# Kernel optimization log

Measured on AMD Instinct MI355X. Metric: run time of the kernel, lower is better.

## Reference

```python
import jax, jax.numpy as jnp
import numpy as np

N = 100000; E = 1000000; D = 192; FD = 64; L = 6; MLP = 192
TW = 768; NPD = 6; CPD = 7; TEMP = 0.5; NREL = 2; EPS = 1e-5


def _ln(x, g, b):
    mu = jnp.mean(x, axis=-1, keepdims=True)
    var = jnp.mean(jnp.square(x - mu), axis=-1, keepdims=True)
    return (x - mu) * jax.lax.rsqrt(var + EPS) * g + b


def _bn(x, g, b):
    # BatchNorm1d in training mode: batch statistics over the N (node) axis
    mu = jnp.mean(x, axis=0, keepdims=True)
    var = jnp.mean(jnp.square(x - mu), axis=0, keepdims=True)
    return (x - mu) * jax.lax.rsqrt(var + EPS) * g + b


def _rgcn(x, Wrel, Wroot, bias, src, dst, etype):
    # PyG RGCNConv, aggr='mean': out_i = x_i @ Wroot + b + sum_r mean_{j in N_r(i)} x_j @ W_r
    out = x @ Wroot + bias
    for r in range(NREL):
        h = x @ Wrel[r]                                   # [N, D] per-relation transform
        mask = (etype == r)
        msg = jnp.where(mask[:, None], jnp.take(h, src, axis=0), 0.0)  # [E, D]
        agg = jax.ops.segment_sum(msg, dst, num_segments=N)
        cnt = jax.ops.segment_sum(mask.astype(x.dtype), dst, num_segments=N)
        out = out + agg / jnp.maximum(cnt, 1.0)[:, None]
    return out


def _forward(tweet, num_prop, comments_prop,
             Wt, bt, Wn, bnum, Wc, bc,
             Wv, bv, Wo, bo, ln1_g, ln1_b, bn_g, bn_b,
             W1, b1, W2, b2, ln2_g, ln2_b,
             Wrel, Wroot, rgcn_b, Wm1, bm1, Wm2, bm2, Wm3, bm3,
             edge_index, edge_type, labels, train_idx):
    lrelu = jax.nn.leaky_relu  # negative_slope=0.01, same as torch LeakyReLU default
    t = lrelu(tweet @ Wt + bt)
    n = lrelu(num_prop @ Wn + bnum)
    c = lrelu(comments_prop @ Wc + bc)
    x = jnp.concatenate([t, n, c], axis=1)  # [N, D]; seq dim of size 1 is elided
    for i in range(L):
        # MHA over seq_len=1: softmax over a single key is exactly 1, so
        # attn_out = out_proj(v_proj(x)); Q/K projections have zero effect/grad.
        v = x @ Wv[i] + bv[i]
        x = x + (v @ Wo[i] + bo[i])          # dropout in eval mode = identity
        x = _ln(x, ln1_g[i], ln1_b[i])
        x = _bn(x, bn_g[i], bn_b[i])
        f = lrelu(x @ W1[i] + b1[i]) @ W2[i] + b2[i]
        x = x + f
        x = _ln(x, ln2_g[i], ln2_b[i])
    # supervised contrastive loss on first train_idx nodes (train_idx static int)
    feat = x[:train_idx]
    lab = labels[:train_idx]
    fn = feat / jnp.linalg.norm(feat, axis=-1, keepdims=True)
    sim = (fn @ fn.T) / TEMP                              # [T, T]
    ex = jnp.exp(sim)
    match = (lab[:, None] == lab[None, :]).astype(x.dtype)
    closs = jnp.mean(-jnp.log(jnp.sum(match * ex, axis=1) / jnp.sum(ex, axis=1)))
    # two passes through the SAME (shared-weight) RGCN; dropout(p=0.1) eval = identity
    src, dst = edge_index[0], edge_index[1]
    h = _rgcn(x, Wrel, Wroot, rgcn_b, src, dst, edge_type)
    h = _rgcn(h, Wrel, Wroot, rgcn_b, src, dst, edge_type)
    h = lrelu(h @ Wm1 + bm1)
    h = lrelu(h @ Wm2 + bm2)
    logits = h @ Wm3 + bm3                                # [N, 2]
    return logits, closs


def setup_inputs() -> dict:
    key = jax.random.key(0)
    ks = iter(jax.random.split(key, 64))
    f32 = jnp.float32
    def p(*shape):
        fan_in = shape[-2] if len(shape) >= 2 else shape[-1]
        return jax.random.normal(next(ks), shape, f32) * (1.0 / np.sqrt(fan_in))
    inp = {
        'tweet': jax.random.normal(next(ks), (N, TW), f32),
        'num_prop': jax.random.normal(next(ks), (N, NPD), f32),
        'comments_prop': jax.random.normal(next(ks), (N, CPD), f32),
        'Wt': p(TW, FD), 'bt': jnp.zeros((FD,), f32),
        'Wn': p(NPD, FD), 'bnum': jnp.zeros((FD,), f32),
        'Wc': p(CPD, FD), 'bc': jnp.zeros((FD,), f32),
        'Wv': p(L, D, D), 'bv': jnp.zeros((L, D), f32),
        'Wo': p(L, D, D), 'bo': jnp.zeros((L, D), f32),
        'ln1_g': jnp.ones((L, D), f32), 'ln1_b': jnp.zeros((L, D), f32),
        'bn_g': jnp.ones((L, D), f32), 'bn_b': jnp.zeros((L, D), f32),
        'W1': p(L, D, MLP), 'b1': jnp.zeros((L, MLP), f32),
        'W2': p(L, MLP, D), 'b2': jnp.zeros((L, D), f32),
        'ln2_g': jnp.ones((L, D), f32), 'ln2_b': jnp.zeros((L, D), f32),
        'Wrel': p(NREL, D, D), 'Wroot': p(D, D), 'rgcn_b': jnp.zeros((D,), f32),
        'Wm1': p(D, MLP), 'bm1': jnp.zeros((MLP,), f32),
        'Wm2': p(MLP, D), 'bm2': jnp.zeros((D,), f32),
        'Wm3': p(D, 2), 'bm3': jnp.zeros((2,), f32),
        'edge_index': jax.random.randint(next(ks), (2, E), 0, N, jnp.int32),
        'edge_type': jax.random.randint(next(ks), (E,), 0, NREL, jnp.int32),
        'labels': jax.random.randint(next(ks), (N,), 0, 2, jnp.int32),
        'train_idx': 8192,
    }
    return inp


def reference(tweet, num_prop, comments_prop, Wt, bt, Wn, bnum, Wc, bc,
              Wv, bv, Wo, bo, ln1_g, ln1_b, bn_g, bn_b,
              W1, b1, W2, b2, ln2_g, ln2_b,
              Wrel, Wroot, rgcn_b, Wm1, bm1, Wm2, bm2, Wm3, bm3,
              edge_index, edge_type, labels, train_idx):
    return _forward(tweet, num_prop, comments_prop, Wt, bt, Wn, bnum, Wc, bc,
                    Wv, bv, Wo, bo, ln1_g, ln1_b, bn_g, bn_b,
                    W1, b1, W2, b2, ln2_g, ln2_b,
                    Wrel, Wroot, rgcn_b, Wm1, bm1, Wm2, bm2, Wm3, bm3,
                    edge_index, edge_type, labels, train_idx)
```

## Files before the change

kernel.cpp:

```cpp
#include <hip/hip_runtime.h>

#define NN 100000
#define EE 1000000
#define DDIM 192
#define NLAYER 6
#define TRAIN 8192
#define SLOPE 0.01f
#define EPS_LN 1e-5f
#define TOTSEG (2 * NN)
#define SCAN_NB 98

typedef float f32x4 __attribute__((ext_vector_type(4)));
typedef __bf16 bf16x8 __attribute__((ext_vector_type(8)));
typedef unsigned short ushort_t;
typedef unsigned int uint_t;

__device__ __forceinline__ float lrelu(float v) { return v > 0.0f ? v : SLOPE * v; }

__device__ __forceinline__ ushort_t f2bf(float f) {
    union { float f; uint_t u; } v; v.f = f;
    uint_t u = v.u;
    u += 0x7fffu + ((u >> 16) & 1u);
    return (ushort_t)(u >> 16);
}

__device__ __forceinline__ float bf2f(ushort_t b) {
    union { uint_t u; float f; } v; v.u = ((uint_t)b) << 16; return v.f;
}

__device__ __forceinline__ float wave_sum(float s) {
    #pragma unroll
    for (int off = 32; off > 0; off >>= 1) s += __shfl_down(s, off);
    return __shfl(s, 0);
}

__global__ __launch_bounds__(256) void prep_w(
    const float* __restrict__ Wt, const float* __restrict__ Wv,
    const float* __restrict__ Wo, const float* __restrict__ W1,
    const float* __restrict__ W2, const float* __restrict__ Wrel,
    const float* __restrict__ Wroot, const float* __restrict__ Wm1,
    const float* __restrict__ Wm2, ushort_t* __restrict__ WTt,
    ushort_t* __restrict__ WTs, ushort_t* __restrict__ WTg)
{
    const int bid = blockIdx.x;
    if (bid < 29 * 144) {
        const int mat = bid / 144;
        const int o = (bid % 144) * 256 + threadIdx.x;
        const float* src;
        if      (mat <  6) src = Wv   + (size_t)mat * 36864;
        else if (mat < 12) src = Wo   + (size_t)(mat - 6)  * 36864;
        else if (mat < 18) src = W1   + (size_t)(mat - 12) * 36864;
        else if (mat < 24) src = W2   + (size_t)(mat - 18) * 36864;
        else if (mat < 26) src = Wrel + (size_t)(mat - 24) * 36864;
        else if (mat == 26) src = Wroot;
        else if (mat == 27) src = Wm1;
        else                src = Wm2;
        const int m = o / 192, k = o - m * 192;
        const ushort_t b = f2bf(src[(size_t)k * 192 + m]);
        if (mat == 24 || mat == 25)
            WTg[(size_t)m * 576 + 192 + (mat - 24) * 192 + k] = b;
        else if (mat == 26)
            WTg[(size_t)m * 576 + k] = b;
        else
            WTs[(size_t)mat * 36864 + o] = b;
    } else {
        const int o = (bid - 29 * 144) * 256 + threadIdx.x;
        const int m = o / 768, k = o - m * 768;
        WTt[o] = f2bf(Wt[(size_t)k * 64 + m]);
    }
}

template <int NFRAG, bool BIAS, bool RELU>
__global__ __launch_bounds__(256) void gemm_mfma(
    const float* __restrict__ A, const ushort_t* __restrict__ WT,
    const float* __restrict__ bias, float* __restrict__ C,
    int n, int K, int ldc)
{
    __shared__ ushort_t As[128 * 32];
    __shared__ ushort_t Ws[NFRAG * 16 * 32];
    const int tid = threadIdx.x;
    const int lane = tid & 63, w = tid >> 6;
    const int quad = lane >> 4, l15 = lane & 15;
    const int row0 = blockIdx.x * 128;

    f32x4 acc[2][NFRAG];
    #pragma unroll
    for (int m = 0; m < 2; ++m)
        #pragma unroll
        for (int nf = 0; nf < NFRAG; ++nf)
            acc[m][nf] = (f32x4){0.f, 0.f, 0.f, 0.f};

    const int srow = tid >> 1, shalf = tid & 1;
    const bool arow_ok = (row0 + srow) < n;
    const float* aptr = A + (size_t)(row0 + srow) * K + shalf * 16;
    const int ktiles = K >> 5;

    float f[16];
    if (arow_ok) {
        const float4* p = (const float4*)aptr;
        #pragma unroll
        for (int i = 0; i < 4; ++i) {
            const float4 t4 = p[i];
            f[i * 4 + 0] = t4.x; f[i * 4 + 1] = t4.y;
            f[i * 4 + 2] = t4.z; f[i * 4 + 3] = t4.w;
        }
    } else {
        #pragma unroll
        for (int i = 0; i < 16; ++i) f[i] = 0.f;
    }

    for (int t = 0; t < ktiles; ++t) {
        const int k0 = t << 5;
        uint_t u[8];
        #pragma unroll
        for (int i = 0; i < 8; ++i)
            u[i] = (uint_t)f2bf(f[2 * i]) | ((uint_t)f2bf(f[2 * i + 1]) << 16);
        uint4* dsta = (uint4*)&As[srow * 32 + shalf * 16];
        dsta[0] = make_uint4(u[0], u[1], u[2], u[3]);
        dsta[1] = make_uint4(u[4], u[5], u[6], u[7]);

        #pragma unroll
        for (int s = tid; s < NFRAG * 64; s += 256) {
            const int col = s >> 2, part = s & 3;
            *(uint4*)&Ws[col * 32 + part * 8] =
                *(const uint4*)(WT + (size_t)col * K + k0 + part * 8);
        }
        __syncthreads();

        float fn_[16];
        const bool more = (t + 1 < ktiles);
        if (more) {
            if (arow_ok) {
                const float4* p = (const float4*)(aptr + k0 + 32);
                #pragma unroll
                for (int i = 0; i < 4; ++i) {
                    const float4 t4 = p[i];
                    fn_[i * 4 + 0] = t4.x; fn_[i * 4 + 1] = t4.y;
                    fn_[i * 4 + 2] = t4.z; fn_[i * 4 + 3] = t4.w;
                }
            } else {
                #pragma unroll
                for (int i = 0; i < 16; ++i) fn_[i] = 0.f;
            }
        }

        const bf16x8 a0 = *(const bf16x8*)&As[(w * 32 + l15) * 32 + quad * 8];
        const bf16x8 a1 = *(const bf16x8*)&As[(w * 32 + 16 + l15) * 32 + quad * 8];
        #pragma unroll
        for (int nf = 0; nf < NFRAG; ++nf) {
            const bf16x8 b = *(const bf16x8*)&Ws[(nf * 16 + l15) * 32 + quad * 8];
            acc[0][nf] = __builtin_amdgcn_mfma_f32_16x16x32_bf16(a0, b, acc[0][nf], 0, 0, 0);
            acc[1][nf] = __builtin_amdgcn_mfma_f32_16x16x32_bf16(a1, b, acc[1][nf], 0, 0, 0);
        }
        __syncthreads();
        if (more) {
            #pragma unroll
            for (int i = 0; i < 16; ++i) f[i] = fn_[i];
        }
    }

    #pragma unroll
    for (int m = 0; m < 2; ++m) {
        #pragma unroll
        for (int reg = 0; reg < 4; ++reg) {
            const int gr = row0 + w * 32 + m * 16 + quad * 4 + reg;
            if (gr >= n) continue;
            #pragma unroll
            for (int nf = 0; nf < NFRAG; ++nf) {
                const int col = nf * 16 + l15;
                float x = acc[m][nf][reg] + (BIAS ? bias[col] : 0.f);
                if (RELU) x = lrelu(x);
                C[(size_t)gr * ldc + col] = x;
            }
        }
    }
}

template <bool ABF, bool RELU1, bool RELU2, bool RES, bool LNORM, bool BN,
          bool BNSTAT, bool CF32, bool CBF>
__global__ __launch_bounds__(256, 2) void gemm2_mfma(
    const void* __restrict__ Ain, const ushort_t* __restrict__ wta,
    const float* __restrict__ bias1, const ushort_t* __restrict__ wtb,
    const float* __restrict__ bias2, const void* __restrict__ resin,
    float* __restrict__ C, ushort_t* __restrict__ Cbf,
    const float* __restrict__ bnsum, const float* __restrict__ bng,
    const float* __restrict__ bnb, float* __restrict__ bnacc,
    const float* __restrict__ lg, const float* __restrict__ lb, int n)
{
    constexpr int VST = 200;
    __shared__ ushort_t Vs[128 * VST];
    __shared__ ushort_t Ws[192 * 32];
    __shared__ float scs[DDIM], shs[DDIM];
    ushort_t* As = Vs;
    const int tid = threadIdx.x;
    const int lane = tid & 63, w = tid >> 6;
    const int quad = lane >> 4, l15 = lane & 15;
    const int row0 = blockIdx.x * 128;

    if constexpr (BN) {
        const float invN = 1.0f / (float)NN;
        for (int j = tid; j < DDIM; j += 256) {
            const float mu = bnsum[j] * invN;
            const float var = bnsum[DDIM + j] * invN - mu * mu;
            const float sc = bng[j] * rsqrtf(var + EPS_LN);
            scs[j] = sc;
            shs[j] = fmaf(-mu, sc, bnb[j]);
        }
        __syncthreads();
    }

    f32x4 acc[2][12];
    #pragma unroll
    for (int m = 0; m < 2; ++m)
        #pragma unroll
        for (int nf = 0; nf < 12; ++nf)
            acc[m][nf] = (f32x4){0.f, 0.f, 0.f, 0.f};

    const int srow = tid >> 1, shalf = tid & 1;
    const bool arow_ok = (row0 + srow) < n;
    const float*    aF = (const float*)Ain + (size_t)(row0 + srow) * DDIM + shalf * 16;
    const ushort_t* aB = (const ushort_t*)Ain + (size_t)(row0 + srow) * DDIM + shalf * 16;

    float f[16];
    uint4 ub[2];

    if constexpr (!ABF) {
        if (arow_ok) {
            const float4* p = (const float4*)aF;
            #pragma unroll
            for (int i = 0; i < 4; ++i) {
                const float4 t4 = p[i];
                f[i * 4 + 0] = t4.x; f[i * 4 + 1] = t4.y;
                f[i * 4 + 2] = t4.z; f[i * 4 + 3] = t4.w;
            }
        } else {
            #pragma unroll
            for (int i = 0; i < 16; ++i) f[i] = 0.f;
        }
    } else {
        if (arow_ok) {
            const uint4* p = (const uint4*)aB;
            ub[0] = p[0]; ub[1] = p[1];
        } else {
            ub[0] = make_uint4(0, 0, 0, 0); ub[1] = make_uint4(0, 0, 0, 0);
        }
    }

    #pragma unroll 1
    for (int t = 0; t < 6; ++t) {
        const int k0 = t << 5;
        uint4* dsta = (uint4*)&As[srow * 32 + shalf * 16];
        if constexpr (!ABF) {
            uint_t u[8];
            #pragma unroll
            for (int i = 0; i < 8; ++i)
                u[i] = (uint_t)f2bf(f[2 * i]) | ((uint_t)f2bf(f[2 * i + 1]) << 16);
            dsta[0] = make_uint4(u[0], u[1], u[2], u[3]);
            dsta[1] = make_uint4(u[4], u[5], u[6], u[7]);
        } else if constexpr (BN) {
            const float4* scp = (const float4*)&scs[k0 + shalf * 16];
            const float4* shp = (const float4*)&shs[k0 + shalf * 16];
            const uint_t* uw = (const uint_t*)ub;
            uint_t u[8];
            #pragma unroll
            for (int i = 0; i < 4; ++i) {
                const float4 sc = scp[i], sh = shp[i];
                float x0 = bf2f((ushort_t)(uw[2 * i] & 0xffffu));
                float x1 = bf2f((ushort_t)(uw[2 * i] >> 16));
                float x2 = bf2f((ushort_t)(uw[2 * i + 1] & 0xffffu));
                float x3 = bf2f((ushort_t)(uw[2 * i + 1] >> 16));
                x0 = fmaf(x0, sc.x, sh.x); x1 = fmaf(x1, sc.y, sh.y);
                x2 = fmaf(x2, sc.z, sh.z); x3 = fmaf(x3, sc.w, sh.w);
                u[2 * i]     = (uint_t)f2bf(x0) | ((uint_t)f2bf(x1) << 16);
                u[2 * i + 1] = (uint_t)f2bf(x2) | ((uint_t)f2bf(x3) << 16);
            }
            dsta[0] = make_uint4(u[0], u[1], u[2], u[3]);
            dsta[1] = make_uint4(u[4], u[5], u[6], u[7]);
        } else {
            dsta[0] = ub[0]; dsta[1] = ub[1];
        }

        #pragma unroll
        for (int s = tid; s < 768; s += 256) {
            const int col = s >> 2, part = s & 3;
            *(uint4*)&Ws[col * 32 + part * 8] =
                *(const uint4*)(wta + (size_t)col * DDIM + k0 + part * 8);
        }
        __syncthreads();

        float fn_[16];
        uint4 ubn[2];
        const bool more = (t < 5);
        if (more) {
            if constexpr (!ABF) {
                if (arow_ok) {
                    const float4* p = (const float4*)(aF + k0 + 32);
                    #pragma unroll
                    for (int i = 0; i < 4; ++i) {
                        const float4 t4 = p[i];
                        fn_[i * 4 + 0] = t4.x; fn_[i * 4 + 1] = t4.y;
                        fn_[i * 4 + 2] = t4.z; fn_[i * 4 + 3] = t4.w;
                    }
                } else {
                    #pragma unroll
                    for (int i = 0; i < 16; ++i) fn_[i] = 0.f;
                }
            } else {
                if (arow_ok) {
                    const uint4* p = (const uint4*)(aB + k0 + 32);
                    ubn[0] = p[0]; ubn[1] = p[1];
                } else {
                    ubn[0] = make_uint4(0, 0, 0, 0); ubn[1] = make_uint4(0, 0, 0, 0);
                }
            }
        }

        const bf16x8 a0 = *(const bf16x8*)&As[(w * 32 + l15) * 32 + quad * 8];
        const bf16x8 a1 = *(const bf16x8*)&As[(w * 32 + 16 + l15) * 32 + quad * 8];
        #pragma unroll
        for (int nf = 0; nf < 12; ++nf) {
            const bf16x8 b = *(const bf16x8*)&Ws[(nf * 16 + l15) * 32 + quad * 8];
            acc[0][nf] = __builtin_amdgcn_mfma_f32_16x16x32_bf16(a0, b, acc[0][nf], 0, 0, 0);
            acc[1][nf] = __builtin_amdgcn_mfma_f32_16x16x32_bf16(a1, b, acc[1][nf], 0, 0, 0);
        }
        __syncthreads();
        if (more) {
            if constexpr (!ABF) {
                #pragma unroll
                for (int i = 0; i < 16; ++i) f[i] = fn_[i];
            } else {
                ub[0] = ubn[0]; ub[1] = ubn[1];
            }
        }
    }

    {
        float b1r[12];
        #pragma unroll
        for (int nf = 0; nf < 12; ++nf) b1r[nf] = bias1[nf * 16 + l15];
        #pragma unroll
        for (int m = 0; m < 2; ++m) {
            #pragma unroll
            for (int reg = 0; reg < 4; ++reg) {
                ushort_t* vrow = &Vs[(w * 32 + m * 16 + quad * 4 + reg) * VST + l15];
                #pragma unroll
                for (int nf = 0; nf < 12; ++nf) {
                    float x = acc[m][nf][reg] + b1r[nf];
                    if (RELU1) x = lrelu(x);
                    vrow[nf * 16] = f2bf(x);
                    acc[m][nf][reg] = 0.f;
                }
            }
        }
    }
    __syncthreads();

    #pragma unroll 1
    for (int t = 0; t < 6; ++t) {
        const int k0 = t << 5;
        #pragma unroll
        for (int s = tid; s < 768; s += 256) {
            const int col = s >> 2, part = s & 3;
            *(uint4*)&Ws[col * 32 + part * 8] =
                *(const uint4*)(wtb + (size_t)col * DDIM + k0 + part * 8);
        }
        __syncthreads();
        const bf16x8 a0 = *(const bf16x8*)&Vs[(w * 32 + l15) * VST + k0 + quad * 8];
        const bf16x8 a1 = *(const bf16x8*)&Vs[(w * 32 + 16 + l15) * VST + k0 + quad * 8];
        #pragma unroll
        for (int nf = 0; nf < 12; ++nf) {
            const bf16x8 b = *(const bf16x8*)&Ws[(nf * 16 + l15) * 32 + quad * 8];
            acc[0][nf] = __builtin_amdgcn_mfma_f32_16x16x32_bf16(a0, b, acc[0][nf], 0, 0, 0);
            acc[1][nf] = __builtin_amdgcn_mfma_f32_16x16x32_bf16(a1, b, acc[1][nf], 0, 0, 0);
        }
        __syncthreads();
    }

    int   col[12];
    float bia[12];
    #pragma unroll
    for (int nf = 0; nf < 12; ++nf) {
        col[nf] = nf * 16 + l15;
        bia[nf] = bias2[col[nf]];
    }
    float rsc[12], rsh[12];
    if constexpr (BN && RES) {
        #pragma unroll
        for (int nf = 0; nf < 12; ++nf) {
            rsc[nf] = scs[col[nf]];
            rsh[nf] = shs[col[nf]];
        }
    }
    float cs[12], cs2[12];
    if constexpr (BNSTAT) {
        #pragma unroll
        for (int nf = 0; nf < 12; ++nf) { cs[nf] = 0.f; cs2[nf] = 0.f; }
    }
    #pragma unroll
    for (int m = 0; m < 2; ++m) {
        #pragma unroll
        for (int reg = 0; reg < 4; ++reg) {
            const int gr = row0 + w * 32 + m * 16 + quad * 4 + reg;
            const bool ok = gr < n;
            float v[12];
            #pragma unroll
            for (int nf = 0; nf < 12; ++nf) {
                float x = acc[m][nf][reg] + bia[nf];
                if constexpr (RES) {
                    float r;
                    if constexpr (ABF)
                        r = ok ? bf2f(((const ushort_t*)resin)[(size_t)gr * DDIM + col[nf]]) : 0.f;
                    else
                        r = ok ? ((const float*)resin)[(size_t)gr * DDIM + col[nf]] : 0.f;
                    if constexpr (BN) r = fmaf(r, rsc[nf], rsh[nf]);
                    x += r;
                }
                v[nf] = x;
            }
            if constexpr (LNORM) {
                float s = 0.f, s2 = 0.f;
                #pragma unroll
                for (int nf = 0; nf < 12; ++nf) { s += v[nf]; s2 = fmaf(v[nf], v[nf], s2); }
                #pragma unroll
                for (int off = 1; off < 16; off <<= 1) {
                    s  += __shfl_xor(s, off);
                    s2 += __shfl_xor(s2, off);
                }
                const float mu = s * (1.0f / DDIM);
                const float var = s2 * (1.0f / DDIM) - mu * mu;
                const float rs = rsqrtf(var + EPS_LN);
                #pragma unroll
                for (int nf = 0; nf < 12; ++nf)
                    v[nf] = fmaf((v[nf] - mu) * rs, lg[col[nf]], lb[col[nf]]);
            }
            #pragma unroll
            for (int nf = 0; nf < 12; ++nf) {
                float x = v[nf];
                if (RELU2) x = lrelu(x);
                if constexpr (BNSTAT) {
                    const float xa = ok ? x : 0.f;
                    cs[nf] += xa;
                    cs2[nf] = fmaf(xa, xa, cs2[nf]);
                }
                if (ok) {
                    if constexpr (CF32) C[(size_t)gr * DDIM + col[nf]] = x;
                    if constexpr (CBF)  Cbf[(size_t)gr * DDIM + col[nf]] = f2bf(x);
                }
            }
        }
    }
    if constexpr (BNSTAT) {
        float* bsA = (float*)Ws;
        float* bsB = bsA + 4 * 192;
        #pragma unroll
        for (int nf = 0; nf < 12; ++nf) {
            cs[nf]  += __shfl_xor(cs[nf], 16);  cs[nf]  += __shfl_xor(cs[nf], 32);
            cs2[nf] += __shfl_xor(cs2[nf], 16); cs2[nf] += __shfl_xor(cs2[nf], 32);
        }
        if (quad == 0) {
            #pragma unroll
            for (int nf = 0; nf < 12; ++nf) {
                bsA[w * 192 + col[nf]] = cs[nf];
                bsB[w * 192 + col[nf]] = cs2[nf];
            }
        }
        __syncthreads();
        if (tid < DDIM) {
            const float s  = bsA[tid] + bsA[192 + tid] + bsA[384 + tid] + bsA[576 + tid];
            const float s2 = bsB[tid] + bsB[192 + tid] + bsB[384 + tid] + bsB[576 + tid];
            atomicAdd(&bnacc[tid], s);
            atomicAdd(&bnacc[DDIM + tid], s2);
        }
    }
}

__global__ __launch_bounds__(256) void gemm_cat(
    const ushort_t* __restrict__ A1, const ushort_t* __restrict__ A2,
    const ushort_t* __restrict__ WT, const float* __restrict__ bias,
    ushort_t* __restrict__ Cbf, int n)
{
    __shared__ ushort_t As[128 * 32];
    __shared__ ushort_t Ws[192 * 32];
    const int tid = threadIdx.x;
    const int lane = tid & 63, w = tid >> 6;
    const int quad = lane >> 4, l15 = lane & 15;
    const int row0 = blockIdx.x * 128;

    f32x4 acc[2][12];
    #pragma unroll
    for (int m = 0; m < 2; ++m)
        #pragma unroll
        for (int nf = 0; nf < 12; ++nf)
            acc[m][nf] = (f32x4){0.f, 0.f, 0.f, 0.f};

    const int srow = tid >> 1, shalf = tid & 1;
    const bool arow_ok = (row0 + srow) < n;
    const ushort_t* a1p = A1 + (size_t)(row0 + srow) * 192 + shalf * 16;
    const ushort_t* a2p = A2 + (size_t)(row0 + srow) * 384 + shalf * 16;

    uint4 u0, u1;
    if (arow_ok) {
        const uint4* p = (const uint4*)a1p;
        u0 = p[0]; u1 = p[1];
    } else {
        u0 = make_uint4(0, 0, 0, 0); u1 = make_uint4(0, 0, 0, 0);
    }

    #pragma unroll 1
    for (int t = 0; t < 18; ++t) {
        uint4* dsta = (uint4*)&As[srow * 32 + shalf * 16];
        dsta[0] = u0;
        dsta[1] = u1;

        #pragma unroll
        for (int s = tid; s < 768; s += 256) {
            const int col = s >> 2, part = s & 3;
            *(uint4*)&Ws[col * 32 + part * 8] =
                *(const uint4*)(WT + (size_t)col * 576 + t * 32 + part * 8);
        }
        __syncthreads();

        uint4 un0, un1;
        const bool more = (t < 17);
        if (more) {
            if (arow_ok) {
                const int tn = t + 1;
                const ushort_t* np = (tn < 6) ? (a1p + tn * 32)
                                              : (a2p + (tn - 6) * 32);
                const uint4* p = (const uint4*)np;
                un0 = p[0]; un1 = p[1];
            } else {
                un0 = make_uint4(0, 0, 0, 0); un1 = make_uint4(0, 0, 0, 0);
            }
        }

        const bf16x8 a0 = *(const bf16x8*)&As[(w * 32 + l15) * 32 + quad * 8];
        const bf16x8 a1 = *(const bf16x8*)&As[(w * 32 + 16 + l15) * 32 + quad * 8];
        #pragma unroll
        for (int nf = 0; nf < 12; ++nf) {
            const bf16x8 b = *(const bf16x8*)&Ws[(nf * 16 + l15) * 32 + quad * 8];
            acc[0][nf] = __builtin_amdgcn_mfma_f32_16x16x32_bf16(a0, b, acc[0][nf], 0, 0, 0);
            acc[1][nf] = __builtin_amdgcn_mfma_f32_16x16x32_bf16(a1, b, acc[1][nf], 0, 0, 0);
        }
        __syncthreads();
        if (more) { u0 = un0; u1 = un1; }
    }

    #pragma unroll
    for (int m = 0; m < 2; ++m) {
        #pragma unroll
        for (int reg = 0; reg < 4; ++reg) {
            const int gr = row0 + w * 32 + m * 16 + quad * 4 + reg;
            if (gr >= n) continue;
            #pragma unroll
            for (int nf = 0; nf < 12; ++nf) {
                const int col = nf * 16 + l15;
                Cbf[(size_t)gr * DDIM + col] = f2bf(acc[m][nf][reg] + bias[col]);
            }
        }
    }
}

__global__ __launch_bounds__(256) void embed_nc_k(
    const float* __restrict__ np_, const float* __restrict__ cp,
    const float* __restrict__ Wn, const float* __restrict__ bnum,
    const float* __restrict__ Wc, const float* __restrict__ bc,
    float* __restrict__ x)
{
    const int idx = blockIdx.x * 256 + threadIdx.x;
    if (idx >= NN * 128) return;
    const int node = idx >> 7;
    const int c = idx & 127;
    float acc;
    if (c < 64) {
        acc = bnum[c];
        #pragma unroll
        for (int k = 0; k < 6; ++k) acc = fmaf(np_[node * 6 + k], Wn[k * 64 + c], acc);
    } else {
        const int cc = c - 64;
        acc = bc[cc];
        #pragma unroll
        for (int k = 0; k < 7; ++k) acc = fmaf(cp[node * 7 + k], Wc[k * 64 + cc], acc);
    }
    x[(size_t)node * DDIM + 64 + c] = lrelu(acc);
}

__global__ __launch_bounds__(256) void fnorm_k(const float* __restrict__ x,
                                               ushort_t* __restrict__ fnb)
{
    const int wave = threadIdx.x >> 6, lane = threadIdx.x & 63;
    const int row = blockIdx.x * 4 + wave;
    if (row >= TRAIN) return;
    const float* xr = x + (size_t)row * DDIM;
    const float v0 = xr[lane], v1 = xr[lane + 64], v2 = xr[lane + 128];
    const float q = wave_sum(v0 * v0 + v1 * v1 + v2 * v2);
    const float inv = 1.0f / sqrtf(q);
    ushort_t* fr = fnb + (size_t)row * DDIM;
    fr[lane]       = f2bf(v0 * inv);
    fr[lane + 64]  = f2bf(v1 * inv);
    fr[lane + 128] = f2bf(v2 * inv);
}

__global__ __launch_bounds__(256) void sim_mfma(const ushort_t* __restrict__ fnb,
    const int* __restrict__ lab, float* __restrict__ row_ex, float* __restrict__ row_mt)
{
    __shared__ ushort_t Ai[128 * 32];
    __shared__ ushort_t Bj[128 * 32];
    __shared__ int Li[128], Lj[128];
    const int tid = threadIdx.x, lane = tid & 63, w = tid >> 6;
    const int quad = lane >> 4, l15 = lane & 15;
    const int i0 = blockIdx.x * 128, j0 = blockIdx.y * 128;
    if (tid < 128) Li[tid] = lab[i0 + tid];
    else           Lj[tid - 128] = lab[j0 + tid - 128];
    const int iw = (w >> 1) * 64, jw = (w & 1) * 64;

    f32x4 acc[4][4];
    #pragma unroll
    for (int m = 0; m < 4; ++m)
        #pragma unroll
        for (int nf = 0; nf < 4; ++nf)
            acc[m][nf] = (f32x4){0.f, 0.f, 0.f, 0.f};

    for (int k0 = 0; k0 < DDIM; k0 += 32) {
        #pragma unroll
        for (int s = tid; s < 512; s += 256) {
            const int row = s >> 2, part = s & 3;
            *(uint4*)&Ai[row * 32 + part * 8] =
                *(const uint4*)(fnb + (size_t)(i0 + row) * DDIM + k0 + part * 8);
            *(uint4*)&Bj[row * 32 + part * 8] =
                *(const uint4*)(fnb + (size_t)(j0 + row) * DDIM + k0 + part * 8);
        }
        __syncthreads();
        bf16x8 a[4], b[4];
        #pragma unroll
        for (int m = 0; m < 4; ++m)
            a[m] = *(const bf16x8*)&Ai[(iw + m * 16 + l15) * 32 + quad * 8];
        #pragma unroll
        for (int nf = 0; nf < 4; ++nf)
            b[nf] = *(const bf16x8*)&Bj[(jw + nf * 16 + l15) * 32 + quad * 8];
        #pragma unroll
        for (int m = 0; m < 4; ++m)
// ... 198 lines not shown
    #pragma unroll
    for (int off = 32; off > 0; off >>= 1) {
        s0 += __shfl_down(s0, off);
        s1 += __shfl_down(s1, off);
    }
    if (lane == 0) {
        out[(size_t)row * 2 + 0] = s0 + bm3[0];
        out[(size_t)row * 2 + 1] = s1 + bm3[1];
    }
}

extern "C" void kernel_launch(void* const* d_in, const int* in_sizes, int n_in,
                              void* d_out, int out_size, void* d_ws, size_t ws_size,
                              hipStream_t stream)
{
    const float* tweet   = (const float*)d_in[0];
    const float* np_     = (const float*)d_in[1];
    const float* cp      = (const float*)d_in[2];
    const float* Wt      = (const float*)d_in[3];
    const float* bt      = (const float*)d_in[4];
    const float* Wn      = (const float*)d_in[5];
    const float* bnum    = (const float*)d_in[6];
    const float* Wc      = (const float*)d_in[7];
    const float* bc      = (const float*)d_in[8];
    const float* Wv      = (const float*)d_in[9];
    const float* bv      = (const float*)d_in[10];
    const float* Wo      = (const float*)d_in[11];
    const float* bo      = (const float*)d_in[12];
    const float* ln1g    = (const float*)d_in[13];
    const float* ln1b    = (const float*)d_in[14];
    const float* bng     = (const float*)d_in[15];
    const float* bnb     = (const float*)d_in[16];
    const float* W1      = (const float*)d_in[17];
    const float* b1      = (const float*)d_in[18];
    const float* W2      = (const float*)d_in[19];
    const float* b2      = (const float*)d_in[20];
    const float* ln2g    = (const float*)d_in[21];
    const float* ln2b    = (const float*)d_in[22];
    const float* Wrel    = (const float*)d_in[23];
    const float* Wroot   = (const float*)d_in[24];
    const float* rgcnb   = (const float*)d_in[25];
    const float* Wm1     = (const float*)d_in[26];
    const float* bm1     = (const float*)d_in[27];
    const float* Wm2     = (const float*)d_in[28];
    const float* bm2     = (const float*)d_in[29];
    const float* Wm3     = (const float*)d_in[30];
    const float* bm3     = (const float*)d_in[31];
    const int*   eidx    = (const int*)d_in[32];
    const int*   esrc    = eidx;
    const int*   edst    = eidx + EE;
    const int*   ety     = (const int*)d_in[33];
    const int*   labels  = (const int*)d_in[34];
    float* out = (float*)d_out;

    float* ws = (float*)d_ws;
    const size_t ND = (size_t)NN * DDIM;
    float* B0    = ws;
    float* B1    = B0 + ND;
    float* B2    = B1 + ND;
    float* B3    = B2 + ND;
    float* ROWEX = B3 + ND;
    float* ROWMT = ROWEX + TRAIN;
    float* BNS   = ROWMT + TRAIN;
    int*   CNTI  = (int*)(BNS + 12 * DDIM);
    int*   OFFS  = CNTI + 2 * NN;
    int*   ELIST = OFFS + 2 * NN;
    int*   PART  = ELIST + EE;
    ushort_t* FNb = (ushort_t*)(PART + 128);
    ushort_t* WTt = FNb + (size_t)TRAIN * DDIM;
    ushort_t* WTs = WTt + 49152;
    ushort_t* WTv    = WTs;
    ushort_t* WTo    = WTs + (size_t)6  * 36864;
    ushort_t* WT1    = WTs + (size_t)12 * 36864;
    ushort_t* WT2    = WTs + (size_t)18 * 36864;
    ushort_t* WTm1   = WTs + (size_t)27 * 36864;
    ushort_t* WTm2   = WTs + (size_t)28 * 36864;
    ushort_t* XBF  = (ushort_t*)B3;
    ushort_t* WTg  = (ushort_t*)B3 + ND;
    ushort_t* X1BF = (ushort_t*)B2;
    ushort_t* AGGB = (ushort_t*)B2;

    const int gx = (NN + 127) / 128;
    const dim3 blk(256);

    prep_w<<<29 * 144 + 192, blk, 0, stream>>>(Wt, Wv, Wo, W1, W2, Wrel, Wroot, Wm1, Wm2, WTt, WTs, WTg);

    hipMemsetAsync(CNTI, 0, 2 * NN * sizeof(int), stream);
    cnt_i_k<<<(EE + 255) / 256, blk, 0, stream>>>(edst, ety, CNTI);
    part_k<<<SCAN_NB, blk, 0, stream>>>(CNTI, PART);
    scanp_k<<<1, 128, 0, stream>>>(PART);
    offs_k<<<SCAN_NB, blk, 0, stream>>>(CNTI, PART, OFFS);
    fill_k<<<(EE + 255) / 256, blk, 0, stream>>>(esrc, edst, ety, OFFS, ELIST);

    gemm_mfma<4, true, true><<<gx, blk, 0, stream>>>(tweet, WTt, bt, B0, NN, 768, DDIM);
    embed_nc_k<<<(NN * 128 + 255) / 256, blk, 0, stream>>>(np_, cp, Wn, bnum, Wc, bc, B0);

    hipMemsetAsync(BNS, 0, 12 * DDIM * sizeof(float), stream);
    for (int i = 0; i < NLAYER; ++i) {
        const size_t wo = (size_t)i * 36864;
        float* bnacc_i = BNS + (size_t)i * 2 * DDIM;
        gemm2_mfma<false, false, false, true, true, false, true, false, true>
            <<<gx, blk, 0, stream>>>(
            B0, WTv + wo, bv + i * DDIM, WTo + wo, bo + i * DDIM, B0,
            nullptr, X1BF, nullptr, nullptr, nullptr, bnacc_i,
            ln1g + i * DDIM, ln1b + i * DDIM, NN);
        if (i < NLAYER - 1)
            gemm2_mfma<true, true, false, true, true, true, false, true, false>
                <<<gx, blk, 0, stream>>>(
                X1BF, WT1 + wo, b1 + i * DDIM, WT2 + wo, b2 + i * DDIM, X1BF,
                B0, nullptr, bnacc_i, bng + i * DDIM, bnb + i * DDIM, nullptr,
                ln2g + i * DDIM, ln2b + i * DDIM, NN);
        else
            gemm2_mfma<true, true, false, true, true, true, false, true, true>
                <<<gx, blk, 0, stream>>>(
                X1BF, WT1 + wo, b1 + i * DDIM, WT2 + wo, b2 + i * DDIM, X1BF,
                B0, XBF, bnacc_i, bng + i * DDIM, bnb + i * DDIM, nullptr,
                ln2g + i * DDIM, ln2b + i * DDIM, NN);
    }

    hipMemsetAsync(ROWEX, 0, 2 * TRAIN * sizeof(float), stream);
    fnorm_k<<<TRAIN / 4, blk, 0, stream>>>(B0, FNb);
    sim_mfma<<<dim3(TRAIN / 128, TRAIN / 128), blk, 0, stream>>>(FNb, labels, ROWEX, ROWMT);
    closs_k<<<1, blk, 0, stream>>>(ROWEX, ROWMT, out + 2 * (size_t)NN);

    gather_bf_k<<<(NN + 3) / 4, blk, 0, stream>>>(XBF, ELIST, OFFS, CNTI, AGGB);
    gemm_cat<<<gx, blk, 0, stream>>>(XBF, AGGB, WTg, rgcnb, XBF, NN);

    gather_bf_k<<<(NN + 3) / 4, blk, 0, stream>>>(XBF, ELIST, OFFS, CNTI, AGGB);
    gemm_cat<<<gx, blk, 0, stream>>>(XBF, AGGB, WTg, rgcnb, XBF, NN);

    gemm2_mfma<true, true, true, false, false, false, false, true, false>
        <<<gx, blk, 0, stream>>>(
        XBF, WTm1, bm1, WTm2, bm2, nullptr, B2, nullptr,
        nullptr, nullptr, nullptr, nullptr, nullptr, nullptr, NN);
    logits_k<<<(NN + 3) / 4, blk, 0, stream>>>(B2, Wm3, bm3, out);
}
```

Baseline: 2.105 ms.

## Double-buffer weight tiles, load A fragments directly to registers, use 512-thread blocks

The fused GEMM kernels (gemm2_mfma, gemm_cat) now run 8 waves per 128-row block, each owning 16 rows instead of 32. A fragments are loaded straight from global memory into registers, skipping the LDS staging of A. Weight K-slices are double-buffered in LDS so the next slice is staged while MFMAs run on the current one, which drops one barrier per iteration. f2bf now uses the native __bf16 conversion, and the BN-stat reduction is widened to 8 waves. The trade-off is weight reuse: each B fragment read from LDS now feeds one MFMA instead of two, and occupancy bounds change to 512x4.

```diff
diff --git a/kernel.cpp b/kernel.cpp
--- a/kernel.cpp
+++ b/kernel.cpp
@@ -18,10 +18,8 @@
 __device__ __forceinline__ float lrelu(float v) { return v > 0.0f ? v : SLOPE * v; }
 
 __device__ __forceinline__ ushort_t f2bf(float f) {
-    union { float f; uint_t u; } v; v.f = f;
-    uint_t u = v.u;
-    u += 0x7fffu + ((u >> 16) & 1u);
-    return (ushort_t)(u >> 16);
+    __bf16 h = (__bf16)f;
+    return __builtin_bit_cast(ushort_t, h);
 }
 
 __device__ __forceinline__ float bf2f(ushort_t b) {
@@ -178,7 +176,7 @@
 
 template <bool ABF, bool RELU1, bool RELU2, bool RES, bool LNORM, bool BN,
           bool BNSTAT, bool CF32, bool CBF>
-__global__ __launch_bounds__(256, 2) void gemm2_mfma(
+__global__ __launch_bounds__(512, 4) void gemm2_mfma(
     const void* __restrict__ Ain, const ushort_t* __restrict__ wta,
     const float* __restrict__ bias1, const ushort_t* __restrict__ wtb,
     const float* __restrict__ bias2, const void* __restrict__ resin,
@@ -189,148 +187,112 @@
 {
     constexpr int VST = 200;
     __shared__ ushort_t Vs[128 * VST];
-    __shared__ ushort_t Ws[192 * 32];
+    __shared__ ushort_t Ws[2][192 * 32];
     __shared__ float scs[DDIM], shs[DDIM];
-    ushort_t* As = Vs;
     const int tid = threadIdx.x;
     const int lane = tid & 63, w = tid >> 6;
     const int quad = lane >> 4, l15 = lane & 15;
     const int row0 = blockIdx.x * 128;
+    const int myrow = row0 + w * 16 + l15;
+    const bool rok = myrow < n;
 
     if constexpr (BN) {
         const float invN = 1.0f / (float)NN;
-        for (int j = tid; j < DDIM; j += 256) {
+        for (int j = tid; j < DDIM; j += 512) {
             const float mu = bnsum[j] * invN;
             const float var = bnsum[DDIM + j] * invN - mu * mu;
             const float sc = bng[j] * rsqrtf(var + EPS_LN);
             scs[j] = sc;
             shs[j] = fmaf(-mu, sc, bnb[j]);
         }
-        __syncthreads();
-    }
-
-    f32x4 acc[2][12];
-    #pragma unroll
-    for (int m = 0; m < 2; ++m)
-        #pragma unroll
-        for (int nf = 0; nf < 12; ++nf)
-            acc[m][nf] = (f32x4){0.f, 0.f, 0.f, 0.f};
-
-    const int srow = tid >> 1, shalf = tid & 1;
-    const bool arow_ok = (row0 + srow) < n;
-    const float*    aF = (const float*)Ain + (size_t)(row0 + srow) * DDIM + shalf * 16;
-    const ushort_t* aB = (const ushort_t*)Ain + (size_t)(row0 + srow) * DDIM + shalf * 16;
-
-    float f[16];
-    uint4 ub[2];
-
-    if constexpr (!ABF) {
-        if (arow_ok) {
-            const float4* p = (const float4*)aF;
+    }
+
+    f32x4 acc[12];
+    #pragma unroll
+    for (int nf = 0; nf < 12; ++nf) acc[nf] = (f32x4){0.f, 0.f, 0.f, 0.f};
+
+    const float*    aF = (const float*)Ain    + (size_t)myrow * DDIM + quad * 8;
+    const ushort_t* aB = (const ushort_t*)Ain + (size_t)myrow * DDIM + quad * 8;
+
+    auto stageW = [&](const ushort_t* wt, int t, int b) {
+        const int k0 = t << 5;
+        for (int s = tid; s < 768; s += 512) {
+            const int col = s >> 2, part = s & 3;
+            *(uint4*)&Ws[b][col * 32 + part * 8] =
+                *(const uint4*)(wt + (size_t)col * DDIM + k0 + part * 8);
+        }
+    };
+    auto loadA = [&](int t, float* fo, uint4& uo) {
+        if constexpr (!ABF) {
+            if (rok) {
+                const float4 p0 = *(const float4*)(aF + t * 32);
+                const float4 p1 = *(const float4*)(aF + t * 32 + 4);
+                fo[0] = p0.x; fo[1] = p0.y; fo[2] = p0.z; fo[3] = p0.w;
+                fo[4] = p1.x; fo[5] = p1.y; fo[6] = p1.z; fo[7] = p1.w;
+            } else {
+                #pragma unroll
+                for (int i = 0; i < 8; ++i) fo[i] = 0.f;
+            }
+        } else {
+            uo = rok ? *(const uint4*)(aB + t * 32) : make_uint4(0u, 0u, 0u, 0u);
+        }
+    };
+    auto makeA = [&](const float* fi, const uint4& ui, int t) -> bf16x8 {
+        if constexpr (!ABF) {
+            union { uint_t u[4]; bf16x8 v; } r;
+            #pragma unroll
+            for (int i = 0; i < 4; ++i)
+                r.u[i] = (uint_t)f2bf(fi[2 * i]) | ((uint_t)f2bf(fi[2 * i + 1]) << 16);
+            return r.v;
+        } else if constexpr (BN) {
+            const int c0 = (t << 5) + quad * 8;
+            const float4 sc0 = *(const float4*)&scs[c0];
+            const float4 sc1 = *(const float4*)&scs[c0 + 4];
+            const float4 sh0 = *(const float4*)&shs[c0];
+            const float4 sh1 = *(const float4*)&shs[c0 + 4];
+            const uint_t* uw = (const uint_t*)&ui;
+            float x[8];
             #pragma unroll
             for (int i = 0; i < 4; ++i) {
-                const float4 t4 = p[i];
-                f[i * 4 + 0] = t4.x; f[i * 4 + 1] = t4.y;
-                f[i * 4 + 2] = t4.z; f[i * 4 + 3] = t4.w;
-            }
+                x[2 * i]     = bf2f((ushort_t)(uw[i] & 0xffffu));
+                x[2 * i + 1] = bf2f((ushort_t)(uw[i] >> 16));
+            }
+            x[0] = fmaf(x[0], sc0.x, sh0.x); x[1] = fmaf(x[1], sc0.y, sh0.y);
+            x[2] = fmaf(x[2], sc0.z, sh0.z); x[3] = fmaf(x[3], sc0.w, sh0.w);
+            x[4] = fmaf(x[4], sc1.x, sh1.x); x[5] = fmaf(x[5], sc1.y, sh1.y);
+            x[6] = fmaf(x[6], sc1.z, sh1.z); x[7] = fmaf(x[7], sc1.w, sh1.w);
+            union { uint_t u[4]; bf16x8 v; } r;
+            #pragma unroll
+            for (int i = 0; i < 4; ++i)
+                r.u[i] = (uint_t)f2bf(x[2 * i]) | ((uint_t)f2bf(x[2 * i + 1]) << 16);
+            return r.v;
         } else {
-            #pragma unroll
-            for (int i = 0; i < 16; ++i) f[i] = 0.f;
-        }
-    } else {
-        if (arow_ok) {
-            const uint4* p = (const uint4*)aB;
-            ub[0] = p[0]; ub[1] = p[1];
-        } else {
-            ub[0] = make_uint4(0, 0, 0, 0); ub[1] = make_uint4(0, 0, 0, 0);
-        }
-    }
-
-    #pragma unroll 1
+            return __builtin_bit_cast(bf16x8, ui);
+        }
+    };
+
+    float fc[8]; uint4 uc;
+    stageW(wta, 0, 0);
+    loadA(0, fc, uc);
+    __syncthreads();
+    #pragma unroll 2
     for (int t = 0; t < 6; ++t) {
-        const int k0 = t << 5;
-        uint4* dsta = (uint4*)&As[srow * 32 + shalf * 16];
-        if constexpr (!ABF) {
-            uint_t u[8];
-            #pragma unroll
-            for (int i = 0; i < 8; ++i)
-                u[i] = (uint_t)f2bf(f[2 * i]) | ((uint_t)f2bf(f[2 * i + 1]) << 16);
-            dsta[0] = make_uint4(u[0], u[1], u[2], u[3]);
-            dsta[1] = make_uint4(u[4], u[5], u[6], u[7]);
-        } else if constexpr (BN) {
-            const float4* scp = (const float4*)&scs[k0 + shalf * 16];
-            const float4* shp = (const float4*)&shs[k0 + shalf * 16];
-            const uint_t* uw = (const uint_t*)ub;
-            uint_t u[8];
-            #pragma unroll
-            for (int i = 0; i < 4; ++i) {
-                const float4 sc = scp[i], sh = shp[i];
-                float x0 = bf2f((ushort_t)(uw[2 * i] & 0xffffu));
-                float x1 = bf2f((ushort_t)(uw[2 * i] >> 16));
-                float x2 = bf2f((ushort_t)(uw[2 * i + 1] & 0xffffu));
-                float x3 = bf2f((ushort_t)(uw[2 * i + 1] >> 16));
-                x0 = fmaf(x0, sc.x, sh.x); x1 = fmaf(x1, sc.y, sh.y);
-                x2 = fmaf(x2, sc.z, sh.z); x3 = fmaf(x3, sc.w, sh.w);
-                u[2 * i]     = (uint_t)f2bf(x0) | ((uint_t)f2bf(x1) << 16);
-                u[2 * i + 1] = (uint_t)f2bf(x2) | ((uint_t)f2bf(x3) << 16);
-            }
-            dsta[0] = make_uint4(u[0], u[1], u[2], u[3]);
-            dsta[1] = make_uint4(u[4], u[5], u[6], u[7]);
-        } else {
-            dsta[0] = ub[0]; dsta[1] = ub[1];
-        }
-
-        #pragma unroll
-        for (int s = tid; s < 768; s += 256) {
-            const int col = s >> 2, part = s & 3;
-            *(uint4*)&Ws[col * 32 + part * 8] =
-                *(const uint4*)(wta + (size_t)col * DDIM + k0 + part * 8);
-        }
-        __syncthreads();
-
-        float fn_[16];
-        uint4 ubn[2];
-        const bool more = (t < 5);
-        if (more) {
-            if constexpr (!ABF) {
-                if (arow_ok) {
-                    const float4* p = (const float4*)(aF + k0 + 32);
-                    #pragma unroll
-                    for (int i = 0; i < 4; ++i) {
-                        const float4 t4 = p[i];
-                        fn_[i * 4 + 0] = t4.x; fn_[i * 4 + 1] = t4.y;
-                        fn_[i * 4 + 2] = t4.z; fn_[i * 4 + 3] = t4.w;
-                    }
-                } else {
-                    #pragma unroll
-                    for (int i = 0; i < 16; ++i) fn_[i] = 0.f;
-                }
-            } else {
-                if (arow_ok) {
-                    const uint4* p = (const uint4*)(aB + k0 + 32);
-                    ubn[0] = p[0]; ubn[1] = p[1];
-                } else {
-                    ubn[0] = make_uint4(0, 0, 0, 0); ubn[1] = make_uint4(0, 0, 0, 0);
-                }
-            }
-        }
-
-        const bf16x8 a0 = *(const bf16x8*)&As[(w * 32 + l15) * 32 + quad * 8];
-        const bf16x8 a1 = *(const bf16x8*)&As[(w * 32 + 16 + l15) * 32 + quad * 8];
+        const int b = t & 1;
+        if (t < 5) stageW(wta, t + 1, b ^ 1);
+        float fn[8]; uint4 un;
+        if (t < 5) loadA(t + 1, fn, un);
+        const bf16x8 a = makeA(fc, uc, t);
         #pragma unroll
         for (int nf = 0; nf < 12; ++nf) {
-            const bf16x8 b = *(const bf16x8*)&Ws[(nf * 16 + l15) * 32 + quad * 8];
-            acc[0][nf] = __builtin_amdgcn_mfma_f32_16x16x32_bf16(a0, b, acc[0][nf], 0, 0, 0);
-            acc[1][nf] = __builtin_amdgcn_mfma_f32_16x16x32_bf16(a1, b, acc[1][nf], 0, 0, 0);
-        }
-        __syncthreads();
-        if (more) {
+            const bf16x8 bb = *(const bf16x8*)&Ws[b][(nf * 16 + l15) * 32 + quad * 8];
+            acc[nf] = __builtin_amdgcn_mfma_f32_16x16x32_bf16(a, bb, acc[nf], 0, 0, 0);
+        }
+        __syncthreads();
+        if (t < 5) {
             if constexpr (!ABF) {
                 #pragma unroll
-                for (int i = 0; i < 16; ++i) f[i] = fn_[i];
-            } else {
-                ub[0] = ubn[0]; ub[1] = ubn[1];
-            }
+                for (int i = 0; i < 8; ++i) fc[i] = fn[i];
+            } else uc = un;
         }
     }
 
@@ -339,39 +301,29 @@
         #pragma unroll
         for (int nf = 0; nf < 12; ++nf) b1r[nf] = bias1[nf * 16 + l15];
         #pragma unroll
-        for (int m = 0; m < 2; ++m) {
-            #pragma unroll
-            for (int reg = 0; reg < 4; ++reg) {
-                ushort_t* vrow = &Vs[(w * 32 + m * 16 + quad * 4 + reg) * VST + l15];
-                #pragma unroll
-                for (int nf = 0; nf < 12; ++nf) {
-                    float x = acc[m][nf][reg] + b1r[nf];
-                    if (RELU1) x = lrelu(x);
-                    vrow[nf * 16] = f2bf(x);
-                    acc[m][nf][reg] = 0.f;
-                }
-            }
-        }
-    }
+        for (int reg = 0; reg < 4; ++reg) {
+            ushort_t* vrow = &Vs[(w * 16 + quad * 4 + reg) * VST + l15];
+            #pragma unroll
+            for (int nf = 0; nf < 12; ++nf) {
+                float x = acc[nf][reg] + b1r[nf];
+                if (RELU1) x = lrelu(x);
+                vrow[nf * 16] = f2bf(x);
+                acc[nf][reg] = 0.f;
+            }
+        }
+    }
+    stageW(wtb, 0, 0);
     __syncthreads();
 
-    #pragma unroll 1
+    #pragma unroll 2
     for (int t = 0; t < 6; ++t) {
-        const int k0 = t << 5;
-        #pragma unroll
-        for (int s = tid; s < 768; s += 256) {
-            const int col = s >> 2, part = s & 3;
-            *(uint4*)&Ws[col * 32 + part * 8] =
-                *(const uint4*)(wtb + (size_t)col * DDIM + k0 + part * 8);
-        }
-        __syncthreads();
-        const bf16x8 a0 = *(const bf16x8*)&Vs[(w * 32 + l15) * VST + k0 + quad * 8];
-        const bf16x8 a1 = *(const bf16x8*)&Vs[(w * 32 + 16 + l15) * VST + k0 + quad * 8];
+        const int b = t & 1;
+        if (t < 5) stageW(wtb, t + 1, b ^ 1);
+        const bf16x8 a = *(const bf16x8*)&Vs[(w * 16 + l15) * VST + (t << 5) + quad * 8];
         #pragma unroll
         for (int nf = 0; nf < 12; ++nf) {
-            const bf16x8 b = *(const bf16x8*)&Ws[(nf * 16 + l15) * 32 + quad * 8];
-            acc[0][nf] = __builtin_amdgcn_mfma_f32_16x16x32_bf16(a0, b, acc[0][nf], 0, 0, 0);
-            acc[1][nf] = __builtin_amdgcn_mfma_f32_16x16x32_bf16(a1, b, acc[1][nf], 0, 0, 0);
+            const bf16x8 bb = *(const bf16x8*)&Ws[b][(nf * 16 + l15) * 32 + quad * 8];
+            acc[nf] = __builtin_amdgcn_mfma_f32_16x16x32_bf16(a, bb, acc[nf], 0, 0, 0);
         }
         __syncthreads();
     }
@@ -397,61 +349,58 @@
         for (int nf = 0; nf < 12; ++nf) { cs[nf] = 0.f; cs2[nf] = 0.f; }
     }
     #pragma unroll
-    for (int m = 0; m < 2; ++m) {
-        #pragma unroll
-        for (int reg = 0; reg < 4; ++reg) {
-            const int gr = row0 + w * 32 + m * 16 + quad * 4 + reg;
-            const bool ok = gr < n;
-            float v[12];
-            #pragma unroll
-            for (int nf = 0; nf < 12; ++nf) {
-                float x = acc[m][nf][reg] + bia[nf];
-                if constexpr (RES) {
-                    float r;
-                    if constexpr (ABF)
-                        r = ok ? bf2f(((const ushort_t*)resin)[(size_t)gr * DDIM + col[nf]]) : 0.f;
-                    else
-                        r = ok ? ((const float*)resin)[(size_t)gr * DDIM + col[nf]] : 0.f;
-                    if constexpr (BN) r = fmaf(r, rsc[nf], rsh[nf]);
-                    x += r;
-                }
-                v[nf] = x;
-            }
-            if constexpr (LNORM) {
-                float s = 0.f, s2 = 0.f;
-                #pragma unroll
-                for (int nf = 0; nf < 12; ++nf) { s += v[nf]; s2 = fmaf(v[nf], v[nf], s2); }
-                #pragma unroll
-                for (int off = 1; off < 16; off <<= 1) {
-                    s  += __shfl_xor(s, off);
-                    s2 += __shfl_xor(s2, off);
-                }
-                const float mu = s * (1.0f / DDIM);
-                const float var = s2 * (1.0f / DDIM) - mu * mu;
-                const float rs = rsqrtf(var + EPS_LN);
-                #pragma unroll
-                for (int nf = 0; nf < 12; ++nf)
-                    v[nf] = fmaf((v[nf] - mu) * rs, lg[col[nf]], lb[col[nf]]);
-            }
-            #pragma unroll
-            for (int nf = 0; nf < 12; ++nf) {
-                float x = v[nf];
-                if (RELU2) x = lrelu(x);
-                if constexpr (BNSTAT) {
-                    const float xa = ok ? x : 0.f;
-                    cs[nf] += xa;
-                    cs2[nf] = fmaf(xa, xa, cs2[nf]);
-                }
-                if (ok) {
-                    if constexpr (CF32) C[(size_t)gr * DDIM + col[nf]] = x;
-                    if constexpr (CBF)  Cbf[(size_t)gr * DDIM + col[nf]] = f2bf(x);
-                }
+    for (int reg = 0; reg < 4; ++reg) {
+        const int gr = row0 + w * 16 + quad * 4 + reg;
+        const bool ok = gr < n;
+        float v[12];
+        #pragma unroll
+        for (int nf = 0; nf < 12; ++nf) {
+            float x = acc[nf][reg] + bia[nf];
+            if constexpr (RES) {
+                float r;
+                if constexpr (ABF)
+                    r = ok ? bf2f(((const ushort_t*)resin)[(size_t)gr * DDIM + col[nf]]) : 0.f;
+                else
+                    r = ok ? ((const float*)resin)[(size_t)gr * DDIM + col[nf]] : 0.f;
+                if constexpr (BN) r = fmaf(r, rsc[nf], rsh[nf]);
+                x += r;
+            }
+            v[nf] = x;
+        }
+        if constexpr (LNORM) {
+            float s = 0.f, s2 = 0.f;
+            #pragma unroll
+            for (int nf = 0; nf < 12; ++nf) { s += v[nf]; s2 = fmaf(v[nf], v[nf], s2); }
+            #pragma unroll
+            for (int off = 1; off < 16; off <<= 1) {
+                s  += __shfl_xor(s, off);
+                s2 += __shfl_xor(s2, off);
+            }
+            const float mu = s * (1.0f / DDIM);
+            const float var = s2 * (1.0f / DDIM) - mu * mu;
+            const float rs = rsqrtf(var + EPS_LN);
+            #pragma unroll
+            for (int nf = 0; nf < 12; ++nf)
+                v[nf] = fmaf((v[nf] - mu) * rs, lg[col[nf]], lb[col[nf]]);
+        }
+        #pragma unroll
+        for (int nf = 0; nf < 12; ++nf) {
+            float x = v[nf];
+            if (RELU2) x = lrelu(x);
+            if constexpr (BNSTAT) {
+                const float xa = ok ? x : 0.f;
+                cs[nf] += xa;
+                cs2[nf] = fmaf(xa, xa, cs2[nf]);
+            }
+            if (ok) {
+                if constexpr (CF32) C[(size_t)gr * DDIM + col[nf]] = x;
+                if constexpr (CBF)  Cbf[(size_t)gr * DDIM + col[nf]] = f2bf(x);
             }
         }
     }
     if constexpr (BNSTAT) {
-        float* bsA = (float*)Ws;
-        float* bsB = bsA + 4 * 192;
+        float* bsA = (float*)&Ws[0][0];
+        float* bsB = bsA + 8 * 192;
         #pragma unroll
         for (int nf = 0; nf < 12; ++nf) {
             cs[nf]  += __shfl_xor(cs[nf], 16);  cs[nf]  += __shfl_xor(cs[nf], 32);
@@ -466,97 +415,81 @@
         }
         __syncthreads();
         if (tid < DDIM) {
-            const float s  = bsA[tid] + bsA[192 + tid] + bsA[384 + tid] + bsA[576 + tid];
-            const float s2 = bsB[tid] + bsB[192 + tid] + bsB[384 + tid] + bsB[576 + tid];
+            float s = 0.f, s2 = 0.f;
+            #pragma unroll
+            for (int k = 0; k < 8; ++k) {
+                s  += bsA[k * 192 + tid];
+                s2 += bsB[k * 192 + tid];
+            }
             atomicAdd(&bnacc[tid], s);
             atomicAdd(&bnacc[DDIM + tid], s2);
         }
     }
 }
 
-__global__ __launch_bounds__(256) void gemm_cat(
+__global__ __launch_bounds__(512, 4) void gemm_cat(
     const ushort_t* __restrict__ A1, const ushort_t* __restrict__ A2,
     const ushort_t* __restrict__ WT, const float* __restrict__ bias,
     ushort_t* __restrict__ Cbf, int n)
 {
-    __shared__ ushort_t As[128 * 32];
-    __shared__ ushort_t Ws[192 * 32];
+    __shared__ ushort_t Ws[2][192 * 32];
     const int tid = threadIdx.x;
     const int lane = tid & 63, w = tid >> 6;
     const int quad = lane >> 4, l15 = lane & 15;
     const int row0 = blockIdx.x * 128;
-
-    f32x4 acc[2][12];
-    #pragma unroll
-    for (int m = 0; m < 2; ++m)
-        #pragma unroll
-        for (int nf = 0; nf < 12; ++nf)
-            acc[m][nf] = (f32x4){0.f, 0.f, 0.f, 0.f};
-
-    const int srow = tid >> 1, shalf = tid & 1;
-    const bool arow_ok = (row0 + srow) < n;
-    const ushort_t* a1p = A1 + (size_t)(row0 + srow) * 192 + shalf * 16;
-    const ushort_t* a2p = A2 + (size_t)(row0 + srow) * 384 + shalf * 16;
-
-    uint4 u0, u1;
-    if (arow_ok) {
-        const uint4* p = (const uint4*)a1p;
-        u0 = p[0]; u1 = p[1];
-    } else {
-        u0 = make_uint4(0, 0, 0, 0); u1 = make_uint4(0, 0, 0, 0);
-    }
-
-    #pragma unroll 1
+    const int myrow = row0 + w * 16 + l15;
+    const bool rok = myrow < n;
+
+    f32x4 acc[12];
+    #pragma unroll
+    for (int nf = 0; nf < 12; ++nf) acc[nf] = (f32x4){0.f, 0.f, 0.f, 0.f};
+
+    const ushort_t* a1p = A1 + (size_t)myrow * 192 + quad * 8;
+    const ushort_t* a2p = A2 + (size_t)myrow * 384 + quad * 8;
+
+    auto stageW = [&](int t, int b) {
+        const int k0 = t << 5;
+        for (int s = tid; s < 768; s += 512) {
+            const int col = s >> 2, part = s & 3;
+            *(uint4*)&Ws[b][col * 32 + part * 8] =
+                *(const uint4*)(WT + (size_t)col * 576 + k0 + part * 8);
+        }
+    };
+    auto loadA = [&](int t) -> uint4 {
+        if (!rok) return make_uint4(0u, 0u, 0u, 0u);
+        const ushort_t* p = (t < 6) ? (a1p + t * 32) : (a2p + (t - 6) * 32);
+        return *(const uint4*)p;
+    };
+
+    uint4 uc;
+    stageW(0, 0);
+    uc = loadA(0);
+    __syncthreads();
+
+    #pragma unroll 2
     for (int t = 0; t < 18; ++t) {
-        uint4* dsta = (uint4*)&As[srow * 32 + shalf * 16];
-        dsta[0] = u0;
-        dsta[1] = u1;
-
-        #pragma unroll
-        for (int s = tid; s < 768; s += 256) {
-            const int col = s >> 2, part = s & 3;
-            *(uint4*)&Ws[col * 32 + part * 8] =
-                *(const uint4*)(WT + (size_t)col * 576 + t * 32 + part * 8);
-        }
-        __syncthreads();
-
-        uint4 un0, un1;
-        const bool more = (t < 17);
-        if (more) {
-            if (arow_ok) {
-                const int tn = t + 1;
-                const ushort_t* np = (tn < 6) ? (a1p + tn * 32)
-                                              : (a2p + (tn - 6) * 32);
-                const uint4* p = (const uint4*)np;
-                un0 = p[0]; un1 = p[1];
-            } else {
-                un0 = make_uint4(0, 0, 0, 0); un1 = make_uint4(0, 0, 0, 0);
-            }
-        }
-
-        const bf16x8 a0 = *(const bf16x8*)&As[(w * 32 + l15) * 32 + quad * 8];
-        const bf16x8 a1 = *(const bf16x8*)&As[(w * 32 + 16 + l15) * 32 + quad * 8];
+        const int b = t & 1;
+        if (t < 17) stageW(t + 1, b ^ 1);
+        uint4 un;
+        if (t < 17) un = loadA(t + 1);
+        const bf16x8 a = __builtin_bit_cast(bf16x8, uc);
         #pragma unroll
         for (int nf = 0; nf < 12; ++nf) {
-            const bf16x8 b = *(const bf16x8*)&Ws[(nf * 16 + l15) * 32 + quad * 8];
-            acc[0][nf] = __builtin_amdgcn_mfma_f32_16x16x32_bf16(a0, b, acc[0][nf], 0, 0, 0);
-            acc[1][nf] = __builtin_amdgcn_mfma_f32_16x16x32_bf16(a1, b, acc[1][nf], 0, 0, 0);
-        }
-        __syncthreads();
-        if (more) { u0 = un0; u1 = un1; }
-    }
-
-    #pragma unroll
-    for (int m = 0; m < 2; ++m) {
-        #pragma unroll
-        for (int reg = 0; reg < 4; ++reg) {
-            const int gr = row0 + w * 32 + m * 16 + quad * 4 + reg;
-            if (gr >= n) continue;
-            #pragma unroll
-            for (int nf = 0; nf < 12; ++nf) {
-                const int col = nf * 16 + l15;
-                Cbf[(size_t)gr * DDIM + col] = f2bf(acc[m][nf][reg] + bias[col]);
-            }
+            const bf16x8 bb = *(const bf16x8*)&Ws[b][(nf * 16 + l15) * 32 + quad * 8];
+            acc[nf] = __builtin_amdgcn_mfma_f32_16x16x32_bf16(a, bb, acc[nf], 0, 0, 0);
+        }
+        __syncthreads();
+        if (t < 17) uc = un;
+    }
+
+    #pragma unroll
+    for (int reg = 0; reg < 4; ++reg) {
+        const int gr = row0 + w * 16 + quad * 4 + reg;
+        if (gr >= n) continue;
+        #pragma unroll
+        for (int nf = 0; nf < 12; ++nf) {
+            const int col = nf * 16 + l15;
+            Cbf[(size_t)gr * DDIM + col] = f2bf(acc[nf][reg] + bias[col]);
         }
     }
 }
@@ -921,6 +854,7 @@
 
     const int gx = (NN + 127) / 128;
     const dim3 blk(256);
+    const dim3 blk5(512);
 
     prep_w<<<29 * 144 + 192, blk, 0, stream>>>(Wt, Wv, Wo, W1, W2, Wrel, Wroot, Wm1, Wm2, WTt, WTs, WTg);
 
@@ -939,19 +873,19 @@
         const size_t wo = (size_t)i * 36864;
         float* bnacc_i = BNS + (size_t)i * 2 * DDIM;
         gemm2_mfma<false, false, false, true, true, false, true, false, true>
-            <<<gx, blk, 0, stream>>>(
+            <<<gx, blk5, 0, stream>>>(
             B0, WTv + wo, bv + i * DDIM, WTo + wo, bo + i * DDIM, B0,
             nullptr, X1BF, nullptr, nullptr, nullptr, bnacc_i,
             ln1g + i * DDIM, ln1b + i * DDIM, NN);
         if (i < NLAYER - 1)
             gemm2_mfma<true, true, false, true, true, true, false, true, false>
-                <<<gx, blk, 0, stream>>>(
+                <<<gx, blk5, 0, stream>>>(
                 X1BF, WT1 + wo, b1 + i * DDIM, WT2 + wo, b2 + i * DDIM, X1BF,
                 B0, nullptr, bnacc_i, bng + i * DDIM, bnb + i * DDIM, nullptr,
                 ln2g + i * DDIM, ln2b + i * DDIM, NN);
         else
             gemm2_mfma<true, true, false, true, true, true, false, true, true>
-                <<<gx, blk, 0, stream>>>(
+                <<<gx, blk5, 0, stream>>>(
                 X1BF, WT1 + wo, b1 + i * DDIM, WT2 + wo, b2 + i * DDIM, X1BF,
                 B0, XBF, bnacc_i, bng + i * DDIM, bnb + i * DDIM, nullptr,
                 ln2g + i * DDIM, ln2b + i * DDIM, NN);
@@ -963,13 +897,13 @@
     closs_k<<<1, blk, 0, stream>>>(ROWEX, ROWMT, out + 2 * (size_t)NN);
 
     gather_bf_k<<<(NN + 3) / 4, blk, 0, stream>>>(XBF, ELIST, OFFS, CNTI, AGGB);
-    gemm_cat<<<gx, blk, 0, stream>>>(XBF, AGGB, WTg, rgcnb, XBF, NN);
+    gemm_cat<<<gx, blk5, 0, stream>>>(XBF, AGGB, WTg, rgcnb, XBF, NN);
 
     gather_bf_k<<<(NN + 3) / 4, blk, 0, stream>>>(XBF, ELIST, OFFS, CNTI, AGGB);
-    gemm_cat<<<gx, blk, 0, stream>>>(XBF, AGGB, WTg, rgcnb, XBF, NN);
+    gemm_cat<<<gx, blk5, 0, stream>>>(XBF, AGGB, WTg, rgcnb, XBF, NN);
 
     gemm2_mfma<true, true, true, false, false, false, false, true, false>
-        <<<gx, blk, 0, stream>>>(
+        <<<gx, blk5, 0, stream>>>(
         XBF, WTm1, bm1, WTm2, bm2, nullptr, B2, nullptr,
         nullptr, nullptr, nullptr, nullptr, nullptr, nullptr, NN);
     logits_k<<<(NN + 3) / 4, blk, 0, stream>>>(B2, Wm3, bm3, out);
```

Measured after the change: 1.894 ms. 1.11x faster.
